# Optimization experiments

Measured on AMD Instinct MI355X. Metric: run time of the kernel, lower is better.

## Reference

```python
import jax, jax.numpy as jnp
import numpy as np

B, I, M, R, C = 2048, 16, 4, 4096, 10  # batch, input_dim, num_mfs, num_rules, num_classes


def setup_inputs() -> dict:
    key = jax.random.key(0)
    k1, k2, k3, k4, k5 = jax.random.split(key, 5)
    x = jax.random.normal(k1, (B, I), dtype=jnp.float32)
    centers = jax.random.normal(k2, (I, M), dtype=jnp.float32)
    widths = jax.random.uniform(k3, (I, M), dtype=jnp.float32, minval=0.5, maxval=1.5)
    consequents = jax.random.normal(k4, (R, I + 1, C), dtype=jnp.float32)
    rule_idx = jax.random.randint(k5, (I, R), 0, M, dtype=jnp.int32)
    return {"x": x, "centers": centers, "widths": widths,
            "consequents": consequents, "rule_idx": rule_idx}


def reference(x, centers, widths, consequents, rule_idx):
    # Gaussian membership functions: [B, I, M] (note: +1e-9 inside exp, as in source)
    mfs = jnp.exp(-(x[:, :, None] - centers[None]) ** 2 / (2.0 * widths[None] ** 2) + 1e-9)
    # Gather per-rule MF values along the M axis: [B, I, R]
    rule_mfs = mfs[:, jnp.arange(I)[:, None], rule_idx]
    # Product t-norm over input dims -> firing strengths [B, R]
    firing = jnp.prod(rule_mfs, axis=1)
    norm_fs = firing / (jnp.sum(firing, axis=1, keepdims=True) + 1e-9)
    # Extended input with bias [B, I+1]
    x_ext = jnp.concatenate([x, jnp.ones((x.shape[0], 1), dtype=x.dtype)], axis=1)
    # Outer product phi [B, R, I+1], then flat GEMM with consequents
    phi = norm_fs[:, :, None] * jax.lax.stop_gradient(x_ext)[:, None, :]
    y_hat = phi.reshape(x.shape[0], R * (I + 1)) @ consequents.reshape(R * (I + 1), C)
    return y_hat, norm_fs, x_ext
```

## Files before the change

### kernel.cpp

```cpp
#include <hip/hip_runtime.h>
#include <stdint.h>

typedef short short8 __attribute__((ext_vector_type(8)));
typedef float f32x4 __attribute__((ext_vector_type(4)));

#define B_ 2048
#define I_ 16
#define M_ 4
#define R_ 4096
#define C_ 10
#define NX 17
#define NW 170
#define NPAD 192
#define KSPLIT 16
#define KCH (R_ / KSPLIT)

#define Y_OFF    0
#define NORM_OFF (B_ * C_)
#define XE_OFF   (B_ * C_ + B_ * R_)

#define PK_OFF    0
#define WT_OFF    16384
#define NFB_OFF   (WT_OFF + NPAD * R_ * 2)
#define PARTY_OFF (NFB_OFF + B_ * R_ * 2)

#define MFMA16(a, b, c) __builtin_amdgcn_mfma_f32_16x16x32_bf16(a, b, c, 0, 0, 0)

__device__ __forceinline__ uint16_t f2bf(float f) {
    uint32_t u = __builtin_bit_cast(uint32_t, f);
    uint32_t r = u + 0x7fffu + ((u >> 16) & 1u);
    return (uint16_t)(r >> 16);
}

__global__ void pack_kernel(const int* __restrict__ rule_idx,
                            uint32_t* __restrict__ packed) {
    int r = blockIdx.x * 256 + threadIdx.x;
    if (r < R_) {
        uint32_t p = 0;
#pragma unroll
        for (int i = 0; i < I_; ++i)
            p |= ((uint32_t)rule_idx[i * R_ + r] & 3u) << (2 * i);
        packed[r] = p;
    }
}

__global__ __launch_bounds__(256) void prep_wt(const float* __restrict__ cons,
                                               uint16_t* __restrict__ wt) {
    int n = blockIdx.x;
    int t = threadIdx.x;
    for (int kk = 0; kk < R_; kk += 256) {
        int k = kk + t;
        uint16_t v = 0;
        if (n < NW) v = f2bf(cons[(size_t)k * NW + n]);
        wt[(size_t)n * R_ + k] = v;
    }
}

__global__ __launch_bounds__(256) void fuzz_kernel(
        const float* __restrict__ x, const float* __restrict__ centers,
        const float* __restrict__ widths, const uint32_t* __restrict__ packed,
        float* __restrict__ out, uint16_t* __restrict__ nfb) {
    int b = blockIdx.x;
    int t = threadIdx.x;
    __shared__ float xs[I_];
    __shared__ float tab[8 * 16];
    __shared__ float wsum[4];

    if (t < I_) xs[t] = x[b * I_ + t];
    if (t < NX) out[XE_OFF + b * NX + t] = (t < I_) ? x[b * I_ + t] : 1.0f;
    __syncthreads();

    if (t < 128) {
        int q  = t >> 4;
        int hi = (t >> 2) & 3;
        int lo = t & 3;
        int i0 = 2 * q, i1 = 2 * q + 1;
        float d0 = xs[i0] - centers[i0 * M_ + lo];
        float w0 = widths[i0 * M_ + lo];
        float m0 = expf(-(d0 * d0) / (2.0f * w0 * w0) + 1e-9f);
        float d1 = xs[i1] - centers[i1 * M_ + hi];
        float w1 = widths[i1 * M_ + hi];
        float m1 = expf(-(d1 * d1) / (2.0f * w1 * w1) + 1e-9f);
        tab[t] = m0 * m1;
    }
    __syncthreads();

    float fs[16];
    float lsum = 0.f;
#pragma unroll
    for (int k = 0; k < 16; ++k) {
        uint32_t p = packed[t + k * 256];
        float f = tab[        p        & 15];
        f *= tab[ 16 + ((p >>  4) & 15)];
        f *= tab[ 32 + ((p >>  8) & 15)];
        f *= tab[ 48 + ((p >> 12) & 15)];
        f *= tab[ 64 + ((p >> 16) & 15)];
        f *= tab[ 80 + ((p >> 20) & 15)];
        f *= tab[ 96 + ((p >> 24) & 15)];
        f *= tab[112 + ((p >> 28) & 15)];
        fs[k] = f;
        lsum += f;
    }
#pragma unroll
    for (int off = 32; off > 0; off >>= 1) lsum += __shfl_down(lsum, off);
    if ((t & 63) == 0) wsum[t >> 6] = lsum;
    __syncthreads();
    float inv = 1.0f / (wsum[0] + wsum[1] + wsum[2] + wsum[3] + 1e-9f);
#pragma unroll
    for (int k = 0; k < 16; ++k) {
        float v = fs[k] * inv;
        out[NORM_OFF + (size_t)b * R_ + t + k * 256] = v;
        nfb[(size_t)b * R_ + t + k * 256] = f2bf(v);
    }
}

__global__ __launch_bounds__(256) void gemm_kernel(
        const uint16_t* __restrict__ nfb,
        const uint16_t* __restrict__ wt,
        const float* __restrict__ xe,
        float* __restrict__ party) {
    int bt  = blockIdx.x;
    int ks  = blockIdx.y;
    int tid = threadIdx.x;
    int wid = tid >> 6;
    int lane = tid & 63;
    int b0 = bt * 64;
    int k0 = ks * KCH;
    int row = lane & 15;
    int kf  = (lane >> 4) * 8;

    f32x4 acc[4][3];
#pragma unroll
    for (int mt = 0; mt < 4; ++mt)
#pragma unroll
        for (int nt = 0; nt < 3; ++nt) acc[mt][nt] = (f32x4){0.f, 0.f, 0.f, 0.f};

    const uint16_t* Ab = nfb + (size_t)(b0 + row) * R_ + k0 + kf;
    const uint16_t* Bb = wt  + (size_t)(wid * 48 + row) * R_ + k0 + kf;

#pragma unroll 2
    for (int kk = 0; kk < KCH; kk += 32) {
        short8 a0 = *(const short8*)(Ab + kk);
        short8 a1 = *(const short8*)(Ab + (size_t)16 * R_ + kk);
        short8 a2 = *(const short8*)(Ab + (size_t)32 * R_ + kk);
        short8 a3 = *(const short8*)(Ab + (size_t)48 * R_ + kk);
        short8 w0 = *(const short8*)(Bb + kk);
        short8 w1 = *(const short8*)(Bb + (size_t)16 * R_ + kk);
        short8 w2 = *(const short8*)(Bb + (size_t)32 * R_ + kk);
        acc[0][0] = MFMA16(a0, w0, acc[0][0]);
        acc[1][0] = MFMA16(a1, w0, acc[1][0]);
        acc[2][0] = MFMA16(a2, w0, acc[2][0]);
        acc[3][0] = MFMA16(a3, w0, acc[3][0]);
        acc[0][1] = MFMA16(a0, w1, acc[0][1]);
        acc[1][1] = MFMA16(a1, w1, acc[1][1]);
        acc[2][1] = MFMA16(a2, w1, acc[2][1]);
        acc[3][1] = MFMA16(a3, w1, acc[3][1]);
        acc[0][2] = MFMA16(a0, w2, acc[0][2]);
        acc[1][2] = MFMA16(a1, w2, acc[1][2]);
        acc[2][2] = MFMA16(a2, w2, acc[2][2]);
        acc[3][2] = MFMA16(a3, w2, acc[3][2]);
    }

    __shared__ float tile[64][NPAD];
#pragma unroll
    for (int mt = 0; mt < 4; ++mt)
#pragma unroll
        for (int nt = 0; nt < 3; ++nt)
#pragma unroll
            for (int j = 0; j < 4; ++j)
                tile[mt * 16 + (lane >> 4) * 4 + j][wid * 48 + nt * 16 + row] =
                    acc[mt][nt][j];
    __syncthreads();

    for (int idx = tid; idx < 64 * C_; idx += 256) {
        int bl = idx / C_;
        int c  = idx - bl * C_;
        float y = tile[bl][I_ * C_ + c];
        const float* xrow = xe + (size_t)(b0 + bl) * NX;
#pragma unroll
        for (int j = 0; j < I_; ++j) y += xrow[j] * tile[bl][j * C_ + c];
        party[((size_t)ks * B_ + b0 + bl) * C_ + c] = y;
    }
}

__global__ __launch_bounds__(256) void finalize_kernel(
        const float* __restrict__ party, float* __restrict__ out) {
    int idx = blockIdx.x * 256 + threadIdx.x;
    if (idx < B_ * C_) {
        float s = 0.f;
#pragma unroll
        for (int ks = 0; ks < KSPLIT; ++ks) s += party[(size_t)ks * B_ * C_ + idx];
        out[Y_OFF + idx] = s;
    }
}

extern "C" void kernel_launch(void* const* d_in, const int* in_sizes, int n_in,
                              void* d_out, int out_size, void* d_ws, size_t ws_size,
                              hipStream_t stream) {
    const float* x       = (const float*)d_in[0];
    const float* centers = (const float*)d_in[1];
    const float* widths  = (const float*)d_in[2];
    const float* cons    = (const float*)d_in[3];
    const int*   ridx    = (const int*)d_in[4];
    float* out = (float*)d_out;

    uint32_t* packed = (uint32_t*)((char*)d_ws + PK_OFF);
    uint16_t* wt     = (uint16_t*)((char*)d_ws + WT_OFF);
    uint16_t* nfb    = (uint16_t*)((char*)d_ws + NFB_OFF);
    float*    party  = (float*)((char*)d_ws + PARTY_OFF);

    pack_kernel<<<dim3((R_ + 255) / 256), dim3(256), 0, stream>>>(ridx, packed);
    prep_wt<<<dim3(NPAD), dim3(256), 0, stream>>>(cons, wt);
    fuzz_kernel<<<dim3(B_), dim3(256), 0, stream>>>(x, centers, widths, packed, out, nfb);
    gemm_kernel<<<dim3(B_ / 64, KSPLIT), dim3(256), 0, stream>>>(
        nfb, wt, out + XE_OFF, party);
    finalize_kernel<<<dim3((B_ * C_ + 255) / 256), dim3(256), 0, stream>>>(party, out);
}
```

Before: 48.10 us.

## Merge prep kernels, compute firing in log domain, double-buffer GEMM loads, raise K-split

Merges rule-index packing and the consequent transpose into one prep launch, and the transpose now goes through shared memory so global reads are coalesced. Firing strengths become a sum of log-memberships taken from 256-entry per-quad tables, followed by one fast exp. This replaces eight multiplies per rule and changes rounding slightly. The GEMM main loop is fully unrolled with register double-buffered loads, the K split is doubled, and launch bounds request 3 blocks per CU. The larger split doubles the partial-sum traffic that the finalize step has to reduce.

```diff
diff --git a/kernel.cpp b/kernel.cpp
--- a/kernel.cpp
+++ b/kernel.cpp
@@ -12,7 +12,7 @@
 #define NX 17
 #define NW 170
 #define NPAD 192
-#define KSPLIT 16
+#define KSPLIT 32
 #define KCH (R_ / KSPLIT)
 
 #define Y_OFF    0
@@ -32,27 +32,36 @@
     return (uint16_t)(r >> 16);
 }
 
-__global__ void pack_kernel(const int* __restrict__ rule_idx,
-                            uint32_t* __restrict__ packed) {
-    int r = blockIdx.x * 256 + threadIdx.x;
-    if (r < R_) {
-        uint32_t p = 0;
-#pragma unroll
-        for (int i = 0; i < I_; ++i)
-            p |= ((uint32_t)rule_idx[i * R_ + r] & 3u) << (2 * i);
-        packed[r] = p;
-    }
-}
-
-__global__ __launch_bounds__(256) void prep_wt(const float* __restrict__ cons,
-                                               uint16_t* __restrict__ wt) {
-    int n = blockIdx.x;
+__global__ __launch_bounds__(256) void prep_kernel(
+        const int* __restrict__ rule_idx, const float* __restrict__ cons,
+        uint32_t* __restrict__ packed, uint16_t* __restrict__ wt) {
     int t = threadIdx.x;
-    for (int kk = 0; kk < R_; kk += 256) {
-        int k = kk + t;
-        uint16_t v = 0;
-        if (n < NW) v = f2bf(cons[(size_t)k * NW + n]);
-        wt[(size_t)n * R_ + k] = v;
+    if (blockIdx.x == 64) {
+        for (int r = t; r < R_; r += 256) {
+            uint32_t p = 0;
+#pragma unroll
+            for (int i = 0; i < I_; ++i)
+                p |= ((uint32_t)rule_idx[i * R_ + r] & 3u) << (2 * i);
+            packed[r] = p;
+        }
+        return;
+    }
+    __shared__ float lt[64][NW + 1];
+    int k0 = blockIdx.x * 64;
+    for (int idx = t; idx < 64 * NW; idx += 256) {
+        int k = idx / NW, n = idx - k * NW;
+        lt[k][n] = cons[(size_t)(k0 + k) * NW + n];
+    }
+    __syncthreads();
+    for (int idx = t; idx < NPAD * 32; idx += 256) {
+        int n = idx >> 5, kp = idx & 31;
+        uint32_t v = 0;
+        if (n < NW) {
+            uint32_t v0 = f2bf(lt[kp * 2][n]);
+            uint32_t v1 = f2bf(lt[kp * 2 + 1][n]);
+            v = v0 | (v1 << 16);
+        }
+        *(uint32_t*)(wt + (size_t)n * R_ + k0 + kp * 2) = v;
     }
 }
 
@@ -63,25 +72,30 @@
     int b = blockIdx.x;
     int t = threadIdx.x;
     __shared__ float xs[I_];
-    __shared__ float tab[8 * 16];
+    __shared__ float zl[64];
+    __shared__ float tab4[4 * 256];
     __shared__ float wsum[4];
 
     if (t < I_) xs[t] = x[b * I_ + t];
     if (t < NX) out[XE_OFF + b * NX + t] = (t < I_) ? x[b * I_ + t] : 1.0f;
     __syncthreads();
 
-    if (t < 128) {
-        int q  = t >> 4;
-        int hi = (t >> 2) & 3;
-        int lo = t & 3;
-        int i0 = 2 * q, i1 = 2 * q + 1;
-        float d0 = xs[i0] - centers[i0 * M_ + lo];
-        float w0 = widths[i0 * M_ + lo];
-        float m0 = expf(-(d0 * d0) / (2.0f * w0 * w0) + 1e-9f);
-        float d1 = xs[i1] - centers[i1 * M_ + hi];
-        float w1 = widths[i1 * M_ + hi];
-        float m1 = expf(-(d1 * d1) / (2.0f * w1 * w1) + 1e-9f);
-        tab[t] = m0 * m1;
+    if (t < 64) {
+        int i = t >> 2, m = t & 3;
+        float d = xs[i] - centers[i * M_ + m];
+        float w = widths[i * M_ + m];
+        zl[t] = -(d * d) / (2.0f * w * w) + 1e-9f;
+    }
+    __syncthreads();
+
+#pragma unroll
+    for (int u = 0; u < 4; ++u) {
+        int idx = t + u * 256;
+        int q = idx >> 8, xq = idx & 255;
+        tab4[idx] = zl[q * 16 +      (xq & 3)]
+                  + zl[q * 16 +  4 + ((xq >> 2) & 3)]
+                  + zl[q * 16 +  8 + ((xq >> 4) & 3)]
+                  + zl[q * 16 + 12 + ((xq >> 6) & 3)];
     }
     __syncthreads();
 
@@ -90,14 +104,11 @@
 #pragma unroll
     for (int k = 0; k < 16; ++k) {
         uint32_t p = packed[t + k * 256];
-        float f = tab[        p        & 15];
-        f *= tab[ 16 + ((p >>  4) & 15)];
-        f *= tab[ 32 + ((p >>  8) & 15)];
-        f *= tab[ 48 + ((p >> 12) & 15)];
-        f *= tab[ 64 + ((p >> 16) & 15)];
-        f *= tab[ 80 + ((p >> 20) & 15)];
-        f *= tab[ 96 + ((p >> 24) & 15)];
-        f *= tab[112 + ((p >> 28) & 15)];
+        float s = tab4[        p         & 255]
+                + tab4[256 + ((p >>  8) & 255)]
+                + tab4[512 + ((p >> 16) & 255)]
+                + tab4[768 + ((p >> 24) & 255)];
+        float f = __expf(s);
         fs[k] = f;
         lsum += f;
     }
@@ -114,7 +125,7 @@
     }
 }
 
-__global__ __launch_bounds__(256) void gemm_kernel(
+__global__ __launch_bounds__(256, 3) void gemm_kernel(
         const uint16_t* __restrict__ nfb,
         const uint16_t* __restrict__ wt,
         const float* __restrict__ xe,
@@ -138,28 +149,30 @@
     const uint16_t* Ab = nfb + (size_t)(b0 + row) * R_ + k0 + kf;
     const uint16_t* Bb = wt  + (size_t)(wid * 48 + row) * R_ + k0 + kf;
 
-#pragma unroll 2
-    for (int kk = 0; kk < KCH; kk += 32) {
-        short8 a0 = *(const short8*)(Ab + kk);
-        short8 a1 = *(const short8*)(Ab + (size_t)16 * R_ + kk);
-        short8 a2 = *(const short8*)(Ab + (size_t)32 * R_ + kk);
-        short8 a3 = *(const short8*)(Ab + (size_t)48 * R_ + kk);
-        short8 w0 = *(const short8*)(Bb + kk);
-        short8 w1 = *(const short8*)(Bb + (size_t)16 * R_ + kk);
-        short8 w2 = *(const short8*)(Bb + (size_t)32 * R_ + kk);
-        acc[0][0] = MFMA16(a0, w0, acc[0][0]);
-        acc[1][0] = MFMA16(a1, w0, acc[1][0]);
-        acc[2][0] = MFMA16(a2, w0, acc[2][0]);
-        acc[3][0] = MFMA16(a3, w0, acc[3][0]);
-        acc[0][1] = MFMA16(a0, w1, acc[0][1]);
-        acc[1][1] = MFMA16(a1, w1, acc[1][1]);
-        acc[2][1] = MFMA16(a2, w1, acc[2][1]);
-        acc[3][1] = MFMA16(a3, w1, acc[3][1]);
-        acc[0][2] = MFMA16(a0, w2, acc[0][2]);
-        acc[1][2] = MFMA16(a1, w2, acc[1][2]);
-        acc[2][2] = MFMA16(a2, w2, acc[2][2]);
-        acc[3][2] = MFMA16(a3, w2, acc[3][2]);
-    }
+    short8 a[2][4], w[2][3];
+#define LOADS(buf, kk)                                                   \
+    do {                                                                 \
+        a[buf][0] = *(const short8*)(Ab + (kk));                         \
+        a[buf][1] = *(const short8*)(Ab + (size_t)16 * R_ + (kk));       \
+        a[buf][2] = *(const short8*)(Ab + (size_t)32 * R_ + (kk));       \
+        a[buf][3] = *(const short8*)(Ab + (size_t)48 * R_ + (kk));       \
+        w[buf][0] = *(const short8*)(Bb + (kk));                         \
+        w[buf][1] = *(const short8*)(Bb + (size_t)16 * R_ + (kk));       \
+        w[buf][2] = *(const short8*)(Bb + (size_t)32 * R_ + (kk));       \
+    } while (0)
+
+    LOADS(0, 0);
+#pragma unroll
+    for (int it = 0; it < KCH / 32; ++it) {
+        int cur = it & 1;
+        if (it + 1 < KCH / 32) LOADS(cur ^ 1, (it + 1) * 32);
+#pragma unroll
+        for (int nt = 0; nt < 3; ++nt)
+#pragma unroll
+            for (int mt = 0; mt < 4; ++mt)
+                acc[mt][nt] = MFMA16(a[cur][mt], w[cur][nt], acc[mt][nt]);
+    }
+#undef LOADS
 
     __shared__ float tile[64][NPAD];
 #pragma unroll
@@ -209,8 +222,7 @@
     uint16_t* nfb    = (uint16_t*)((char*)d_ws + NFB_OFF);
     float*    party  = (float*)((char*)d_ws + PARTY_OFF);
 
-    pack_kernel<<<dim3((R_ + 255) / 256), dim3(256), 0, stream>>>(ridx, packed);
-    prep_wt<<<dim3(NPAD), dim3(256), 0, stream>>>(cons, wt);
+    prep_kernel<<<dim3(65), dim3(256), 0, stream>>>(ridx, cons, packed, wt);
     fuzz_kernel<<<dim3(B_), dim3(256), 0, stream>>>(x, centers, widths, packed, out, nfb);
     gemm_kernel<<<dim3(B_ / 64, KSPLIT), dim3(256), 0, stream>>>(
         nfb, wt, out + XE_OFF, party);
```

Result: faster. 47.12 us (-2.0%).
